# Optimization experiments

Measured on AMD Instinct MI355X. Metric: run time of the kernel, lower is better.

The kernel has to match this reference:

```python
import jax, jax.numpy as jnp
import numpy as np

B, S, E, H = 2, 2048, 1024, 16
DK = E // H  # 64


def setup_inputs() -> dict:
    key = jax.random.key(0)
    ks = jax.random.split(key, 5)
    scale = 1.0 / np.sqrt(E)
    return {
        "x": jax.random.normal(ks[0], (B, S, E), dtype=jnp.float32),
        "Wq": jax.random.normal(ks[1], (E, E), dtype=jnp.float32) * scale,
        "Wk": jax.random.normal(ks[2], (E, E), dtype=jnp.float32) * scale,
        "Wv": jax.random.normal(ks[3], (E, E), dtype=jnp.float32) * scale,
        "Wo": jax.random.normal(ks[4], (E, E), dtype=jnp.float32) * scale,
    }


def reference(x, Wq, Wk, Wv, Wo):
    # Linear layers: y = x @ W.T (torch nn.Linear convention, bias=False)
    b, s, e = x.shape
    q = (x @ Wq.T).reshape(b, s, H, DK)  # (B,S,H,dk)
    k = (x @ Wk.T).reshape(b, s, H, DK)
    v = (x @ Wv.T).reshape(b, s, H, DK)
    # scores = Q K^T / sqrt(d_k)  -> (B,H,Sq,Sk)
    scores = jnp.einsum("bihd,bkhd->bhik", q, k) / jnp.sqrt(jnp.asarray(DK, x.dtype))
    p = jax.nn.softmax(scores, axis=-1)
    # dropout is identity in eval/deterministic mode
    attn = jnp.einsum("bhik,bkhd->bihd", p, v)  # (B,S,H,dk)
    concat = attn.reshape(b, s, e)
    return concat @ Wo.T
```

## Files before the change

### kernel.cpp

```cpp
#include <hip/hip_runtime.h>
#include <hip/hip_bf16.h>
#include <cstdint>
#include <cstddef>

typedef __bf16 bf16_t;
typedef __attribute__((ext_vector_type(8))) __bf16 bf16x8;
typedef __attribute__((ext_vector_type(4))) __bf16 bf16x4;
typedef __attribute__((ext_vector_type(4))) float f32x4;
typedef __attribute__((ext_vector_type(16))) float f32x16;
typedef uint32_t u32;
typedef __attribute__((ext_vector_type(4))) u32 u32x4;
typedef __attribute__((ext_vector_type(2))) u32 u32x2;

constexpr int B_ = 2, S_ = 2048, E_ = 1024, H_ = 16, DK_ = 64;

__device__ __forceinline__ void gl2lds16(const void* g, void* l) {
  __builtin_amdgcn_global_load_lds(
      (const __attribute__((address_space(1))) void*)g,
      (__attribute__((address_space(3))) void*)l, 16, 0, 0);
}

__device__ __forceinline__ float exp2_(float x) {
#if __has_builtin(__builtin_amdgcn_exp2f)
  return __builtin_amdgcn_exp2f(x);
#else
  return exp2f(x);
#endif
}

__device__ __forceinline__ u32 cvtpk(float lo, float hi) {
  u32 r;
  asm("v_cvt_pk_bf16_f32 %0, %1, %2" : "=v"(r) : "v"(lo), "v"(hi));
  return r;
}

__device__ __forceinline__ void pl32swap(u32& a, u32& b) {
#if __has_builtin(__builtin_amdgcn_permlane32_swap)
  const u32x2 r = __builtin_amdgcn_permlane32_swap(a, b, false, false);
  a = r[0]; b = r[1];
#else
  asm volatile("v_permlane32_swap_b32 %0, %1" : "+v"(a), "+v"(b));
#endif
}

__device__ __forceinline__ bf16x8 ldsfrag(const char* base, int row, int chunk) {
  return *reinterpret_cast<const bf16x8*>(base + row * 128 + (((chunk ^ (row & 7))) << 4));
}

__global__ __launch_bounds__(256) void f2bf_all(const float* __restrict__ x,
                                                const float* __restrict__ w0,
                                                const float* __restrict__ w1,
                                                const float* __restrict__ w2,
                                                const float* __restrict__ w3,
                                                bf16_t* __restrict__ out) {
  const int i = blockIdx.x * 256 + threadIdx.x;
  const float* src;
  int off;
  if (i < (1 << 20)) {
    src = x; off = i;
  } else {
    const int j = i - (1 << 20);
    const int s = j >> 18;
    off = j & 262143;
    src = s == 0 ? w0 : s == 1 ? w1 : s == 2 ? w2 : w3;
  }
  const float4 v = reinterpret_cast<const float4*>(src)[off];
  bf16x4 o;
  o[0] = (bf16_t)v.x; o[1] = (bf16_t)v.y; o[2] = (bf16_t)v.z; o[3] = (bf16_t)v.w;
  reinterpret_cast<bf16x4*>(out)[i] = o;
}

__global__ __launch_bounds__(512) void gemm_qkv(const bf16_t* __restrict__ A,
                                                const bf16_t* __restrict__ Bt,
                                                bf16_t* __restrict__ Qo,
                                                bf16_t* __restrict__ Ko,
                                                bf16_t* __restrict__ Vto,
                                                float qscale) {
  __shared__ bf16_t As[2][256 * 32];
  __shared__ bf16_t Bs[2][256 * 32];
  const int tid = threadIdx.x;
  const int w = tid >> 6, l = tid & 63;
  const int wr = w >> 2, wc = w & 3;
  const int tm = blockIdx.x * 256, tn = blockIdx.y * 256;
  constexpr int K = 1024, nk = K / 32;
  f32x4 acc[8][4] = {};

  auto stage = [&](int k0, int buf) {
    const int c = k0 + (l & 3) * 8;
    const int rb = w * 32;
#pragma unroll
    for (int j = 0; j < 2; ++j) {
      const int r = rb + j * 16;
      gl2lds16(A + (size_t)(tm + r + (l >> 2)) * K + c, As[buf] + r * 32);
      gl2lds16(Bt + (size_t)(tn + r + (l >> 2)) * K + c, Bs[buf] + r * 32);
    }
  };

  stage(0, 0);
  stage(32, 1);

  for (int t = 0; t < nk; ++t) {
    const int cur = t & 1;
    if (t + 1 < nk) asm volatile("s_waitcnt vmcnt(4)" ::: "memory");
    else            asm volatile("s_waitcnt vmcnt(0)" ::: "memory");
    __builtin_amdgcn_s_barrier();
    __builtin_amdgcn_sched_barrier(0);

    bf16x8 af[8], bfr[4];
#pragma unroll
    for (int mi = 0; mi < 8; ++mi)
      af[mi] = *reinterpret_cast<const bf16x8*>(
          As[cur] + (wr * 128 + mi * 16 + (l & 15)) * 32 + (l >> 4) * 8);
#pragma unroll
    for (int ni = 0; ni < 4; ++ni)
      bfr[ni] = *reinterpret_cast<const bf16x8*>(
          Bs[cur] + (wc * 64 + ni * 16 + (l & 15)) * 32 + (l >> 4) * 8);
#pragma unroll
    for (int mi = 0; mi < 8; ++mi)
#pragma unroll
      for (int ni = 0; ni < 4; ++ni)
        acc[mi][ni] =
            __builtin_amdgcn_mfma_f32_16x16x32_bf16(af[mi], bfr[ni], acc[mi][ni], 0, 0, 0);

    if (t + 2 < nk) {
      __builtin_amdgcn_s_barrier();
      __builtin_amdgcn_sched_barrier(0);
      stage((t + 2) * 32, cur);
    }
  }

#pragma unroll
  for (int mi = 0; mi < 8; ++mi)
#pragma unroll
    for (int ni = 0; ni < 4; ++ni) {
      if (tn < 2048) {
        bf16_t* C = (tn < 1024) ? Qo : Ko;
        const float sc = (tn < 1024) ? qscale : 1.0f;
        const int colb = tn & 1023;
#pragma unroll
        for (int r = 0; r < 4; ++r) {
          const int row = tm + wr * 128 + mi * 16 + (l >> 4) * 4 + r;
          const int col = colb + wc * 64 + ni * 16 + (l & 15);
          C[(size_t)row * 1024 + col] = (bf16_t)(acc[mi][ni][r] * sc);
        }
      } else {
        const int tok0 = tm + wr * 128 + mi * 16 + (l >> 4) * 4;
        const int feat = (tn - 2048) + wc * 64 + ni * 16 + (l & 15);
        const int b = tok0 >> 11, s = tok0 & 2047;
        bf16x4 o4;
#pragma unroll
        for (int r = 0; r < 4; ++r) o4[r] = (bf16_t)acc[mi][ni][r];
        *reinterpret_cast<bf16x4*>(Vto + (((size_t)(b * E_ + feat)) << 11) + s) = o4;
      }
    }
}

__global__ __launch_bounds__(256) void gemm_o(const bf16_t* __restrict__ A,
                                              const bf16_t* __restrict__ Bt,
                                              float* __restrict__ C) {
  __shared__ bf16_t As[2][64 * 32];
  __shared__ bf16_t Bs[2][128 * 32];
  const int tid = threadIdx.x;
  const int w = tid >> 6, l = tid & 63;
  const int wr = w >> 1, wc = w & 1;
  const int tm = blockIdx.x * 64, tn = blockIdx.y * 128;
  constexpr int K = 1024, nk = K / 32;
  f32x4 acc[2][4] = {};

  auto stage = [&](int k0, int buf) {
    const int c = k0 + (l & 3) * 8;
    gl2lds16(A + (size_t)(tm + w * 16 + (l >> 2)) * K + c, As[buf] + (w * 16) * 32);
#pragma unroll
    for (int i = 0; i < 2; ++i)
      gl2lds16(Bt + (size_t)(tn + i * 64 + w * 16 + (l >> 2)) * K + c,
               Bs[buf] + (i * 64 + w * 16) * 32);
  };

  stage(0, 0);
  stage(32, 1);

  for (int t = 0; t < nk; ++t) {
    const int cur = t & 1;
    if (t + 1 < nk) asm volatile("s_waitcnt vmcnt(3)" ::: "memory");
    else            asm volatile("s_waitcnt vmcnt(0)" ::: "memory");
    __builtin_amdgcn_s_barrier();
    __builtin_amdgcn_sched_barrier(0);

    bf16x8 af[2], bfr[4];
#pragma unroll
    for (int mi = 0; mi < 2; ++mi)
      af[mi] = *reinterpret_cast<const bf16x8*>(
          As[cur] + (wr * 32 + mi * 16 + (l & 15)) * 32 + (l >> 4) * 8);
#pragma unroll
    for (int ni = 0; ni < 4; ++ni)
      bfr[ni] = *reinterpret_cast<const bf16x8*>(
          Bs[cur] + (wc * 64 + ni * 16 + (l & 15)) * 32 + (l >> 4) * 8);
#pragma unroll
    for (int mi = 0; mi < 2; ++mi)
#pragma unroll
      for (int ni = 0; ni < 4; ++ni)
        acc[mi][ni] =
            __builtin_amdgcn_mfma_f32_16x16x32_bf16(af[mi], bfr[ni], acc[mi][ni], 0, 0, 0);

    if (t + 2 < nk) {
      __builtin_amdgcn_s_barrier();
      __builtin_amdgcn_sched_barrier(0);
      stage((t + 2) * 32, cur);
    }
  }

#pragma unroll
  for (int mi = 0; mi < 2; ++mi)
#pragma unroll
    for (int ni = 0; ni < 4; ++ni)
#pragma unroll
      for (int r = 0; r < 4; ++r) {
        const int row = tm + wr * 32 + mi * 16 + (l >> 4) * 4 + r;
        const int col = tn + wc * 64 + ni * 16 + (l & 15);
        C[(size_t)row * 1024 + col] = acc[mi][ni][r];
      }
}

template <int NSPL>
__global__ __launch_bounds__(256, 2) void attn_fwd(const bf16_t* __restrict__ Q,
                                                   const bf16_t* __restrict__ K,
                                                   const bf16_t* __restrict__ Vt,
                                                   bf16_t* __restrict__ O,
                                                   u32* __restrict__ Op,
                                                   float* __restrict__ lbuf) {
  __shared__ __align__(16) char smem[32768];
  const int tid = threadIdx.x;
  const int w = tid >> 6, l = tid & 63;
  const int hi = l >> 5, l31 = l & 31;
  const int nblk = 512 * NSPL;
  const int flat = blockIdx.x;
  const int wid = (flat & 7) * (nblk >> 3) + (flat >> 3);
  const int qb = wid & 15, bh = (wid >> 4) & 31;
  const int part = wid >> 9;
  const int q0 = qb * 128 + w * 32;
  const size_t hb = (size_t)(bh >> 4) * (S_ * E_) + (size_t)(bh & 15) * DK_;
  const bf16_t* const Qh = Q + hb;
  const bf16_t* const Kh = K + hb;
  const bf16_t* const Vth = Vt + (size_t)bh * (DK_ * S_);

  const int srow = l >> 3;
  const int schunk = (l & 7) ^ srow;

  bf16x8 ones;
  {
    u32x4 ow;
    ow[0] = 0x3F803F80u; ow[1] = 0x3F803F80u; ow[2] = 0x3F803F80u; ow[3] = 0x3F803F80u;
    ones = __builtin_bit_cast(bf16x8, ow);
  }
  f32x16 m12;
#pragma unroll
  for (int u = 0; u < 16; ++u) m12[u] = -12.0f;

  bf16x8 qf[4];
#pragma unroll
  for (int df = 0; df < 4; ++df)
    qf[df] = *reinterpret_cast<const bf16x8*>(
        Qh + (size_t)(q0 + l31) * E_ + df * 16 + hi * 8);

  f32x16 oacc[2] = {};
  f32x16 lacc = {};

  auto stage = [&](int t, int buf) {
    const int t0 = t * 64;
#pragma unroll
    for (int i = 0; i < 2; ++i) {
      const int rg = w * 2 + i;
      const int row = rg * 8 + srow;
      gl2lds16(Kh + (size_t)(t0 + row) * E_ + schunk * 8,
               smem + buf * 8192 + rg * 1024);
      gl2lds16(Vth + (size_t)row * S_ + t0 + schunk * 8,
               smem + 16384 + buf * 8192 + rg * 1024);
    }
  };

  const int ntl = 32 / NSPL;
  const int tbeg = part * ntl;

  stage(tbeg, 0);
  stage(tbeg + 1, 1);

  for (int tt = 0; tt < ntl; ++tt) {
    const int cur = tt & 1;
    if (tt + 1 < ntl) asm volatile("s_waitcnt vmcnt(4)" ::: "memory");
    else              asm volatile("s_waitcnt vmcnt(0)" ::: "memory");
    __builtin_amdgcn_s_barrier();
    __builtin_amdgcn_sched_barrier(0);

    const char* const Kcur = smem + cur * 8192;
    const char* const Vcur = smem + 16384 + cur * 8192;

    f32x16 sacc[2];
    __builtin_amdgcn_s_setprio(1);
#pragma unroll
    for (int kb = 0; kb < 2; ++kb) {
      {
        const bf16x8 kf = ldsfrag(Kcur, kb * 32 + l31, hi);
        sacc[kb] = __builtin_amdgcn_mfma_f32_32x32x16_bf16(kf, qf[0], m12, 0, 0, 0);
      }
#pragma unroll
      for (int df = 1; df < 4; ++df) {
        const bf16x8 kf = ldsfrag(Kcur, kb * 32 + l31, df * 2 + hi);
        sacc[kb] = __builtin_amdgcn_mfma_f32_32x32x16_bf16(kf, qf[df], sacc[kb], 0, 0, 0);
      }
    }
    __builtin_amdgcn_s_setprio(0);

#pragma unroll
    for (int kb = 0; kb < 2; ++kb)
#pragma unroll
      for (int u = 0; u < 16; ++u)
        sacc[kb][u] = exp2_(sacc[kb][u]);

#pragma unroll
    for (int kf = 0; kf < 4; ++kf) {
      const int kb = kf >> 1, u0 = (kf & 1) * 8;
      u32 w0 = cvtpk(sacc[kb][u0 + 0], sacc[kb][u0 + 1]);
      u32 w1 = cvtpk(sacc[kb][u0 + 2], sacc[kb][u0 + 3]);
      u32 w2 = cvtpk(sacc[kb][u0 + 4], sacc[kb][u0 + 5]);
      u32 w3 = cvtpk(sacc[kb][u0 + 6], sacc[kb][u0 + 7]);
      pl32swap(w0, w2);
      pl32swap(w1, w3);
      u32x4 pw; pw[0] = w0; pw[1] = w1; pw[2] = w2; pw[3] = w3;
      const bf16x8 pa = __builtin_bit_cast(bf16x8, pw);
      __builtin_amdgcn_s_setprio(1);
#pragma unroll
      for (int dn = 0; dn < 2; ++dn) {
        const bf16x8 vf = ldsfrag(Vcur, dn * 32 + l31, kf * 2 + hi);
        oacc[dn] = __builtin_amdgcn_mfma_f32_32x32x16_bf16(pa, vf, oacc[dn], 0, 0, 0);
      }
      lacc = __builtin_amdgcn_mfma_f32_32x32x16_bf16(pa, ones, lacc, 0, 0, 0);
      __builtin_amdgcn_s_setprio(0);
    }

    if (tt + 2 < ntl) {
      __builtin_amdgcn_s_barrier();
      __builtin_amdgcn_sched_barrier(0);
      stage(tbeg + tt + 2, cur);
    }
  }

  if constexpr (NSPL > 1) {
    const int pb = part * 65536 + bh * S_;
#pragma unroll
    for (int u = 0; u < 16; ++u) {
      if (l31 == u) {
        const int q = q0 + (u & 3) + 8 * (u >> 2) + 4 * hi;
        lbuf[pb + q] = lacc[u];
      }
    }
    u32* const Oph = Op + (size_t)part * 2097152 + (size_t)(bh * S_) * 32 + l31;
#pragma unroll
    for (int u = 0; u < 16; ++u) {
      const int q = q0 + (u & 3) + 8 * (u >> 2) + 4 * hi;
      Oph[(size_t)q * 32] = cvtpk(oacc[0][u], oacc[1][u]);
    }
  } else {
#pragma unroll
    for (int u = 0; u < 16; ++u) {
      const float inv = 1.f / lacc[u];
      const int q = q0 + (u & 3) + 8 * (u >> 2) + 4 * hi;
      O[hb + (size_t)q * E_ + l31] = (bf16_t)(oacc[0][u] * inv);
      O[hb + (size_t)q * E_ + 32 + l31] = (bf16_t)(oacc[1][u] * inv);
    }
  }
}

__global__ __launch_bounds__(256) void attn_combine(const u32* __restrict__ Op,
                                                    const float* __restrict__ lbuf,
                                                    bf16_t* __restrict__ Ac) {
  const int idx = blockIdx.x * 256 + threadIdx.x;
  const int r = idx >> 5, c = idx & 31;
  const float lsum = lbuf[r] + lbuf[65536 + r];
  float o0 = 0.f, o1 = 0.f;
#pragma unroll
  for (int i = 0; i < 2; ++i) {
    const u32 p = Op[(size_t)i * 2097152 + (size_t)r * 32 + c];
    o0 += __builtin_bit_cast(float, p << 16);
    o1 += __builtin_bit_cast(float, p & 0xFFFF0000u);
  }
  const float inv = 1.f / lsum;
  const int q = r & 2047, bh = r >> 11;
  bf16_t* const base =
      Ac + (size_t)(bh >> 4) * (S_ * E_) + (size_t)q * E_ + (bh & 15) * DK_;
  base[c] = (bf16_t)(o0 * inv);
  base[c + 32] = (bf16_t)(o1 * inv);
}

extern "C" void kernel_launch(void* const* d_in, const int* in_sizes, int n_in,
                              void* d_out, int out_size, void* d_ws, size_t ws_size,
                              hipStream_t stream) {
  const float* x  = (const float*)d_in[0];
  const float* Wq = (const float*)d_in[1];
  const float* Wk = (const float*)d_in[2];
  const float* Wv = (const float*)d_in[3];
  const float* Wo = (const float*)d_in[4];
  float* out = (float*)d_out;

  bf16_t* xb  = (bf16_t*)d_ws;
  bf16_t* wqb = xb + 4194304;
  bf16_t* wob = wqb + 3145728;
  bf16_t* Qb  = wqb + 4194304;
  bf16_t* Kb  = Qb + 4194304;
  bf16_t* Vtb = Kb + 4194304;
  u32*    Opart = (u32*)(Vtb + 4194304);
  float*  lbuf  = (float*)d_ws;

  const bool split = ws_size >= 76546048ull;

  f2bf_all<<<8192, 256, 0, stream>>>(x, Wq, Wk, Wv, Wo, xb);

  gemm_qkv<<<dim3(16, 12), 512, 0, stream>>>(xb, wqb, Qb, Kb, Vtb, 0.18033688f);

  if (split) {
    bf16_t* Ac = Kb;
    attn_fwd<2><<<1024, 256, 0, stream>>>(Qb, Kb, Vtb, nullptr, Opart, lbuf);
    attn_combine<<<8192, 256, 0, stream>>>(Opart, lbuf, Ac);
    gemm_o<<<dim3(64, 8), 256, 0, stream>>>(Ac, wob, out);
  } else {
    bf16_t* Ac = xb;
    attn_fwd<1><<<512, 256, 0, stream>>>(Qb, Kb, Vtb, Ac, nullptr, nullptr);
    gemm_o<<<dim3(64, 8), 256, 0, stream>>>(Ac, wob, out);
  }
}
```

Measured before the change: 130.0 us.

## Restructure QKV GEMM into 8-phase ping-pong pipeline with XOR-swizzled LDS halves

Rewrites the fused QKV GEMM main loop to use K-tiles of 64 split into A/B half-tiles across two stages (128KB LDS), with an XOR swizzle on the LDS chunk index to avoid bank conflicts. Each iteration runs eight phases that each load fragments for one quadrant, issue the next half-tile's global-to-LDS loads, then run MFMAs at raised priority, interleaving memory traffic with compute. The cost is much larger LDS usage (one block per CU) and more barriers per K step. It also relies on an ldsfrag helper that is not visible here.

```diff
diff --git a/kernel.cpp b/kernel.cpp
--- a/kernel.cpp
+++ b/kernel.cpp
@@ -76,80 +76,105 @@
                                                 bf16_t* __restrict__ Ko,
                                                 bf16_t* __restrict__ Vto,
                                                 float qscale) {
-  __shared__ bf16_t As[2][256 * 32];
-  __shared__ bf16_t Bs[2][256 * 32];
+  __shared__ __align__(16) char smem[131072];
   const int tid = threadIdx.x;
   const int w = tid >> 6, l = tid & 63;
   const int wr = w >> 2, wc = w & 3;
   const int tm = blockIdx.x * 256, tn = blockIdx.y * 256;
-  constexpr int K = 1024, nk = K / 32;
+  const int srow = l >> 3;
+  const int schunk = (l & 7) ^ srow;
+
+  auto aH = [&](int s, int h) -> char* { return smem + (s * 2 + h) * 16384; };
+  auto bH = [&](int s, int h) -> char* { return smem + 65536 + (s * 2 + h) * 16384; };
+
+  auto stageh = [&](const bf16_t* Gbase, char* lds, int kt) {
+#pragma unroll
+    for (int j = 0; j < 2; ++j)
+      gl2lds16(Gbase + (size_t)(w * 16 + j * 8 + srow) * 1024 + kt * 64 + schunk * 8,
+               lds + (w * 2 + j) * 1024);
+  };
+
   f32x4 acc[8][4] = {};
 
-  auto stage = [&](int k0, int buf) {
-    const int c = k0 + (l & 3) * 8;
-    const int rb = w * 32;
-#pragma unroll
-    for (int j = 0; j < 2; ++j) {
-      const int r = rb + j * 16;
-      gl2lds16(A + (size_t)(tm + r + (l >> 2)) * K + c, As[buf] + r * 32);
-      gl2lds16(Bt + (size_t)(tn + r + (l >> 2)) * K + c, Bs[buf] + r * 32);
-    }
-  };
-
-  stage(0, 0);
-  stage(32, 1);
-
-  for (int t = 0; t < nk; ++t) {
-    const int cur = t & 1;
-    if (t + 1 < nk) asm volatile("s_waitcnt vmcnt(4)" ::: "memory");
-    else            asm volatile("s_waitcnt vmcnt(0)" ::: "memory");
+  auto phase = [&](int s, int qa, int qb, auto stagefn, int vmode) {
+    bf16x8 af[4][2], bfv[2][2];
+#pragma unroll
+    for (int m = 0; m < 4; ++m)
+#pragma unroll
+      for (int ks = 0; ks < 2; ++ks)
+        af[m][ks] = ldsfrag(aH(s, qa), wr * 64 + m * 16 + (l & 15), ks * 4 + (l >> 4));
+#pragma unroll
+    for (int n = 0; n < 2; ++n)
+#pragma unroll
+      for (int ks = 0; ks < 2; ++ks)
+        bfv[n][ks] = ldsfrag(bH(s, qb), wc * 32 + n * 16 + (l & 15), ks * 4 + (l >> 4));
+    stagefn();
+    __builtin_amdgcn_s_barrier();
+    asm volatile("s_waitcnt lgkmcnt(0)" ::: "memory");
+    __builtin_amdgcn_sched_barrier(0);
+    __builtin_amdgcn_s_setprio(1);
+#pragma unroll
+    for (int m = 0; m < 4; ++m)
+#pragma unroll
+      for (int n = 0; n < 2; ++n)
+#pragma unroll
+        for (int ks = 0; ks < 2; ++ks)
+          acc[qa * 4 + m][qb * 2 + n] = __builtin_amdgcn_mfma_f32_16x16x32_bf16(
+              af[m][ks], bfv[n][ks], acc[qa * 4 + m][qb * 2 + n], 0, 0, 0);
+    __builtin_amdgcn_s_setprio(0);
+    if (vmode == 1) asm volatile("s_waitcnt vmcnt(4)" ::: "memory");
+    if (vmode == 2) asm volatile("s_waitcnt vmcnt(0)" ::: "memory");
     __builtin_amdgcn_s_barrier();
     __builtin_amdgcn_sched_barrier(0);
-
-    bf16x8 af[8], bfr[4];
-#pragma unroll
-    for (int mi = 0; mi < 8; ++mi)
-      af[mi] = *reinterpret_cast<const bf16x8*>(
-          As[cur] + (wr * 128 + mi * 16 + (l & 15)) * 32 + (l >> 4) * 8);
-#pragma unroll
-    for (int ni = 0; ni < 4; ++ni)
-      bfr[ni] = *reinterpret_cast<const bf16x8*>(
-          Bs[cur] + (wc * 64 + ni * 16 + (l & 15)) * 32 + (l >> 4) * 8);
-#pragma unroll
-    for (int mi = 0; mi < 8; ++mi)
-#pragma unroll
-      for (int ni = 0; ni < 4; ++ni)
-        acc[mi][ni] =
-            __builtin_amdgcn_mfma_f32_16x16x32_bf16(af[mi], bfr[ni], acc[mi][ni], 0, 0, 0);
-
-    if (t + 2 < nk) {
-      __builtin_amdgcn_s_barrier();
-      __builtin_amdgcn_sched_barrier(0);
-      stage((t + 2) * 32, cur);
-    }
-  }
-
-#pragma unroll
-  for (int mi = 0; mi < 8; ++mi)
-#pragma unroll
-    for (int ni = 0; ni < 4; ++ni) {
+  };
+
+  const bf16_t* const A0p = A + (size_t)tm * 1024;
+  const bf16_t* const A1p = A + (size_t)(tm + 128) * 1024;
+  const bf16_t* const B0p = Bt + (size_t)tn * 1024;
+  const bf16_t* const B1p = Bt + (size_t)(tn + 128) * 1024;
+
+  stageh(A0p, aH(0, 0), 0);
+  stageh(B0p, bH(0, 0), 0);
+  stageh(A1p, aH(0, 1), 0);
+  stageh(B1p, bH(0, 1), 0);
+  stageh(B0p, bH(1, 0), 1);
+  stageh(A1p, aH(1, 1), 1);
+  asm volatile("s_waitcnt vmcnt(4)" ::: "memory");
+  __builtin_amdgcn_s_barrier();
+  __builtin_amdgcn_sched_barrier(0);
+
+  for (int t = 0; t < 8; ++t) {
+    const int k1 = 2 * t + 1, ka = 2 * t + 2, kb = 2 * t + 3;
+    const bool va = ka < 16, vb = kb < 16;
+    phase(0, 0, 0, [&] { stageh(A0p, aH(1, 0), k1); stageh(B1p, bH(1, 1), k1); }, 0);
+    phase(0, 1, 0, [&] {}, 0);
+    phase(0, 1, 1, [&] { if (va) stageh(B0p, bH(0, 0), ka); }, 0);
+    phase(0, 0, 1, [&] { if (va) stageh(A1p, aH(0, 1), ka); }, va ? 1 : 2);
+    phase(1, 0, 0, [&] { if (va) stageh(A0p, aH(0, 0), ka); }, 0);
+    phase(1, 1, 0, [&] { if (va) stageh(B1p, bH(0, 1), ka); }, 0);
+    phase(1, 1, 1, [&] { if (vb) stageh(B0p, bH(1, 0), kb); }, 0);
+    phase(1, 0, 1, [&] { if (vb) stageh(A1p, aH(1, 1), kb); }, (t < 7) ? 1 : 0);
+  }
+
+#pragma unroll
+  for (int m = 0; m < 8; ++m)
+#pragma unroll
+    for (int n = 0; n < 4; ++n) {
+      const int row0 = tm + (m >> 2) * 128 + wr * 64 + (m & 3) * 16 + (l >> 4) * 4;
+      const int coll = (n >> 1) * 128 + wc * 32 + (n & 1) * 16 + (l & 15);
       if (tn < 2048) {
         bf16_t* C = (tn < 1024) ? Qo : Ko;
         const float sc = (tn < 1024) ? qscale : 1.0f;
-        const int colb = tn & 1023;
-#pragma unroll
-        for (int r = 0; r < 4; ++r) {
-          const int row = tm + wr * 128 + mi * 16 + (l >> 4) * 4 + r;
-          const int col = colb + wc * 64 + ni * 16 + (l & 15);
-          C[(size_t)row * 1024 + col] = (bf16_t)(acc[mi][ni][r] * sc);
-        }
+        const int col = (tn & 1023) + coll;
+#pragma unroll
+        for (int r = 0; r < 4; ++r)
+          C[(size_t)(row0 + r) * 1024 + col] = (bf16_t)(acc[m][n][r] * sc);
       } else {
-        const int tok0 = tm + wr * 128 + mi * 16 + (l >> 4) * 4;
-        const int feat = (tn - 2048) + wc * 64 + ni * 16 + (l & 15);
-        const int b = tok0 >> 11, s = tok0 & 2047;
+        const int feat = (tn - 2048) + coll;
+        const int b = row0 >> 11, s = row0 & 2047;
         bf16x4 o4;
 #pragma unroll
-        for (int r = 0; r < 4; ++r) o4[r] = (bf16_t)acc[mi][ni][r];
+        for (int r = 0; r < 4; ++r) o4[r] = (bf16_t)acc[m][n][r];
         *reinterpret_cast<bf16x4*>(Vto + (((size_t)(b * E_ + feat)) << 11) + s) = o4;
       }
     }
```

New measurement: 122.4 us. 5.9% less time.
